# Optimization experiments

Hardware: AMD Instinct MI355X
Metric: run time of the kernel (lower is better)

The kernel has to match this reference:

```python
import jax, jax.numpy as jnp
import numpy as np


def setup_inputs() -> dict:
    key = jax.random.key(0)
    kh, ks, kwi, kwo, kcw = jax.random.split(key, 5)
    B = 2048        # decode batch (one token per request)
    H = 2048        # hidden_size
    K = 4           # conv kernel; L_cache = K - 1 = 3
    P = 8192        # req_to_token_pool size
    hidden_states = jax.random.normal(kh, (B, H), dtype=jnp.float32)
    conv_state = jax.random.normal(ks, (P, H, K - 1), dtype=jnp.float32)
    # unique, in-range pool slots (index_copy_ semantics need uniqueness)
    req_pool_indices = jnp.arange(B, dtype=jnp.int32)
    w_in = jax.random.normal(kwi, (3 * H, H), dtype=jnp.float32) * 0.02
    w_out = jax.random.normal(kwo, (H, H), dtype=jnp.float32) * 0.02
    conv_w = jax.random.normal(kcw, (H, K), dtype=jnp.float32) * 0.2
    return {
        "hidden_states": hidden_states,
        "conv_state": conv_state,
        "req_pool_indices": req_pool_indices,
        "w_in": w_in,
        "w_out": w_out,
        "conv_w": conv_w,
    }


def reference(hidden_states, conv_state, req_pool_indices, w_in, w_out, conv_w):
    """Lfm2ShortConv._forward_decode (conv_bias=False).

    Returns (y, new_conv_state) where new_conv_state is the scattered cache.
    """
    idx = req_pool_indices.astype(jnp.int32)
    # in_proj: [B, H] @ [H, 3H] -> [B, 3H]
    proj = hidden_states @ w_in.T
    B_gate, C_gate, x = jnp.split(proj, 3, axis=-1)
    Bx = B_gate * x                                  # [B, H]
    cur = conv_state[idx]                            # gather: [B, H, K-1]
    # sliding window: [old state (K-1 taps), newest token] -> [B, H, K]
    conv_in = jnp.concatenate([cur, Bx[:, :, None]], axis=-1)
    # depthwise causal conv as mul-sum over taps
    conv_out = jnp.einsum("bhk,hk->bh", conv_in, conv_w)
    y = (C_gate * conv_out) @ w_out.T                # [B, H]
    # scatter updated window (drop oldest tap)
    new_conv_state = conv_state.at[idx].set(conv_in[:, :, 1:])
    return y, new_conv_state
```

## Files before the change

### kernel.cpp

```cpp
#include <hip/hip_runtime.h>
#include <hip/hip_bf16.h>


typedef __bf16 bf16x8 __attribute__((ext_vector_type(8)));
typedef float f32x4 __attribute__((ext_vector_type(4)));

__device__ __forceinline__ unsigned short f2bf(float f) {
    union { float f; unsigned int u; } c; c.f = f;
    unsigned int u = c.u;
    u = u + 0x7FFFu + ((u >> 16) & 1u);
    return (unsigned short)(u >> 16);
}
__device__ __forceinline__ float bf2f(unsigned short u) {
    union { unsigned int i; float f; } c; c.i = ((unsigned int)u) << 16;
    return c.f;
}

__global__ void prep(const float4* __restrict__ hs, const float4* __restrict__ wi,
                     const float4* __restrict__ wo,
                     ushort4* __restrict__ hs_bf, ushort4* __restrict__ wi_bf,
                     ushort4* __restrict__ wo_bf,
                     int* __restrict__ inv, int P,
                     int n1, int n2, int n3) {
    int i = blockIdx.x * blockDim.x + threadIdx.x;
    if (i < P) inv[i] = -1;
    const float4* s; ushort4* d; int j = i;
    if (j < n1)            { s = hs; d = hs_bf; }
    else if ((j -= n1) < n2) { s = wi; d = wi_bf; }
    else if ((j -= n2) < n3) { s = wo; d = wo_bf; }
    else return;
    float4 v = s[j];
    ushort4 o; o.x = f2bf(v.x); o.y = f2bf(v.y); o.z = f2bf(v.z); o.w = f2bf(v.w);
    d[j] = o;
}

__global__ void scatter_inv(const int* __restrict__ idx, int* __restrict__ inv, int B) {
    int b = blockIdx.x * blockDim.x + threadIdx.x;
    if (b < B) inv[idx[b]] = b;
}


#define GTILE 128
#define GBK 64

__device__ __forceinline__ void gl_lds16(const unsigned short* g, unsigned short* l) {
    __builtin_amdgcn_global_load_lds(
        (const __attribute__((address_space(1))) unsigned int*)g,
        (__attribute__((address_space(3))) unsigned int*)l,
        16, 0, 0);
}

template<int OUTBF16>
__global__ __launch_bounds__(256) void gemm_bt(
    const unsigned short* __restrict__ A,
    const unsigned short* __restrict__ B,
    void* __restrict__ Cv,
    int M, int N, int K, int ksplit)
{
    __shared__ __align__(16) unsigned short Asm[GTILE * GBK];
    __shared__ __align__(16) unsigned short Bsm[GTILE * GBK];

    const int tid  = threadIdx.x;
    const int lane = tid & 63;
    const int wave = tid >> 6;
    const int quad = lane >> 4;
    const int l16  = lane & 15;

    const int bm = blockIdx.y * GTILE;
    const int bn = blockIdx.x * GTILE;
    const int kb = blockIdx.z * ksplit;

    const int wm = (wave >> 1) * 64;
    const int wn = (wave & 1) * 64;

    f32x4 acc[4][4] = {};

    const int sr = tid >> 3;
    const int scsw = (((tid & 7) ^ (sr & 7)) * 8);
    const unsigned short* Ag[4];
    const unsigned short* Bg[4];
#pragma unroll
    for (int k4 = 0; k4 < 4; k4++) {
        Ag[k4] = A + (size_t)(bm + k4 * 32 + sr) * K + scsw;
        Bg[k4] = B + (size_t)(bn + k4 * 32 + sr) * K + scsw;
    }

    for (int kt = kb; kt < kb + ksplit; kt += GBK) {
        __syncthreads();
#pragma unroll
        for (int k4 = 0; k4 < 4; k4++) {
            gl_lds16(Ag[k4] + kt, Asm + k4 * 2048 + wave * 512);
            gl_lds16(Bg[k4] + kt, Bsm + k4 * 2048 + wave * 512);
        }
        __syncthreads();

#pragma unroll
        for (int kk = 0; kk < 2; kk++) {
            bf16x8 a[4], b[4];
            const int csw = (kk * 32 + quad * 8) ^ ((l16 & 7) * 8);
#pragma unroll
            for (int i = 0; i < 4; i++)
                a[i] = *(const bf16x8*)&Asm[(wm + i * 16 + l16) * GBK + csw];
#pragma unroll
            for (int j = 0; j < 4; j++)
                b[j] = *(const bf16x8*)&Bsm[(wn + j * 16 + l16) * GBK + csw];
#pragma unroll
            for (int i = 0; i < 4; i++)
#pragma unroll
                for (int j = 0; j < 4; j++)
                    acc[i][j] = __builtin_amdgcn_mfma_f32_16x16x32_bf16(
                        a[i], b[j], acc[i][j], 0, 0, 0);
        }
    }

#pragma unroll
    for (int i = 0; i < 4; i++) {
#pragma unroll
        for (int j = 0; j < 4; j++) {
#pragma unroll
            for (int r = 0; r < 4; r++) {
                int row = bm + wm + i * 16 + quad * 4 + r;
                int col = bn + wn + j * 16 + l16;
                if (OUTBF16) {
                    ((unsigned short*)Cv)[(size_t)row * N + col] = f2bf(acc[i][j][r]);
                } else {
                    float* Cp = (float*)Cv + (size_t)blockIdx.z * M * N;
                    Cp[(size_t)row * N + col] = acc[i][j][r];
                }
            }
        }
    }
}

__global__ void elemwise(const unsigned short* __restrict__ proj,
                         const float* __restrict__ cs_in,
                         const int* __restrict__ idx,
                         const float* __restrict__ conv_w,
                         float* __restrict__ state_out,
                         unsigned short* __restrict__ g_bf,
                         int B, int H, int hshift, int hmask)
{
    int t = blockIdx.x * blockDim.x + threadIdx.x;
    if (t >= B * H) return;
    int b = t >> hshift;
    int h = t & hmask;
    int slot = idx[b];
    size_t prow = (size_t)b * 3 * H;
    float Bg = bf2f(proj[prow + h]);
    float Cg = bf2f(proj[prow + H + h]);
    float xv = bf2f(proj[prow + 2 * H + h]);
    float bx = Bg * xv;
    const float* cs = cs_in + ((size_t)slot * H + h) * 3;
    float c0 = cs[0], c1 = cs[1], c2 = cs[2];
    float4 cw = *(const float4*)(conv_w + 4 * h);
    float co = c0 * cw.x + c1 * cw.y + c2 * cw.z + bx * cw.w;
    float* so = state_out + ((size_t)slot * H + h) * 3;
    so[0] = c1; so[1] = c2; so[2] = bx;
    g_bf[t] = f2bf(Cg * co);
}

__global__ __launch_bounds__(256) void writeback(
    const float* __restrict__ cs_in,
    const int* __restrict__ inv,
    float* __restrict__ cs_out,
    int HL)
{
    int p = blockIdx.x;
    if (inv[p] >= 0) return;
    const float4* s4 = (const float4*)(cs_in + (size_t)p * HL);
    float4* d4 = (float4*)(cs_out + (size_t)p * HL);
    int n4 = HL / 4;
    for (int f = threadIdx.x; f < n4; f += blockDim.x) d4[f] = s4[f];
}

__global__ void reduce2(const float4* __restrict__ p0, const float4* __restrict__ p1,
                        float4* __restrict__ y, int n4) {
    int i = blockIdx.x * blockDim.x + threadIdx.x;
    if (i >= n4) return;
    float4 a = p0[i], b = p1[i];
    float4 o; o.x = a.x + b.x; o.y = a.y + b.y; o.z = a.z + b.z; o.w = a.w + b.w;
    y[i] = o;
}

extern "C" void kernel_launch(void* const* d_in, const int* in_sizes, int n_in,
                              void* d_out, int out_size, void* d_ws, size_t ws_size,
                              hipStream_t stream) {
    const float* hs         = (const float*)d_in[0];
    const float* conv_state = (const float*)d_in[1];
    const int*   idx        = (const int*)d_in[2];
    const float* w_in       = (const float*)d_in[3];
    const float* w_out      = (const float*)d_in[4];
    const float* conv_w     = (const float*)d_in[5];

    const int B  = in_sizes[2];
    const int H  = in_sizes[0] / B;
    const int Kc = in_sizes[5] / H;
    const int Lc = Kc - 1;
    const int P  = (int)((long long)in_sizes[1] / ((long long)H * Lc));

    float* y_out     = (float*)d_out;
    float* state_out = y_out + (size_t)B * H;

    unsigned short* hs_bf    = (unsigned short*)d_ws;
    unsigned short* w_in_bf  = hs_bf + (size_t)B * H;
    unsigned short* w_out_bf = w_in_bf + (size_t)3 * H * H;
    unsigned short* proj_bf  = w_out_bf + (size_t)H * H;
    unsigned short* g_bf     = proj_bf + (size_t)B * 3 * H;
    float*          part     = (float*)(g_bf + (size_t)B * H);
    int*            inv      = (int*)(part + (size_t)2 * B * H);

    const int thr = 256;

    {
        int n1 = B * H / 4, n2 = 3 * H * H / 4, n3 = H * H / 4;
        int tot = n1 + n2 + n3;
        prep<<<(tot + thr - 1) / thr, thr, 0, stream>>>(
            (const float4*)hs, (const float4*)w_in, (const float4*)w_out,
            (ushort4*)hs_bf, (ushort4*)w_in_bf, (ushort4*)w_out_bf,
            inv, P, n1, n2, n3);
    }
    scatter_inv<<<(B + thr - 1) / thr, thr, 0, stream>>>(idx, inv, B);

    {
        dim3 grid(3 * H / GTILE, B / GTILE, 1);
        gemm_bt<1><<<grid, 256, 0, stream>>>(hs_bf, w_in_bf, proj_bf, B, 3 * H, H, H);
    }

    {
        int hshift = 0; while ((1 << hshift) < H) hshift++;
        int n = B * H;
        elemwise<<<(n + thr - 1) / thr, thr, 0, stream>>>(
            proj_bf, conv_state, idx, conv_w, state_out, g_bf, B, H, hshift, H - 1);
    }

    writeback<<<P, 256, 0, stream>>>(conv_state, inv, state_out, 3 * H);

    {
        dim3 grid(H / GTILE, B / GTILE, 2);
        gemm_bt<0><<<grid, 256, 0, stream>>>(g_bf, w_out_bf, part, B, H, H, H / 2);
        int n4 = B * H / 4;
        reduce2<<<(n4 + thr - 1) / thr, thr, 0, stream>>>(
            (const float4*)part, (const float4*)(part + (size_t)B * H),
            (float4*)y_out, n4);
    }
}
```

Measured before the change: 502.8 us.

## Fuse state writeback into in-proj GEMM and use atomic split-K for out-proj

The separate writeback kernel is removed. Every fifth block of the in_proj GEMM grid now copies the untouched conv_state slots, so that memory traffic overlaps with MFMA work. The out_proj GEMM switches to 4-way split-K with relaxed float atomics into y, which prep now zero-fills, and the partial buffer and reduce kernel are dropped. This cuts launches and partial-buffer traffic, at the cost of atomic contention, nondeterministic summation order, and copy blocks that may load-imbalance the GEMM.

```diff
diff --git a/kernel.cpp b/kernel.cpp
--- a/kernel.cpp
+++ b/kernel.cpp
@@ -20,14 +20,16 @@
                      const float4* __restrict__ wo,
                      ushort4* __restrict__ hs_bf, ushort4* __restrict__ wi_bf,
                      ushort4* __restrict__ wo_bf,
+                     float4* __restrict__ y,
                      int* __restrict__ inv, int P,
-                     int n1, int n2, int n3) {
+                     int n1, int n2, int n3, int n4) {
     int i = blockIdx.x * blockDim.x + threadIdx.x;
     if (i < P) inv[i] = -1;
     const float4* s; ushort4* d; int j = i;
     if (j < n1)            { s = hs; d = hs_bf; }
     else if ((j -= n1) < n2) { s = wi; d = wi_bf; }
     else if ((j -= n2) < n3) { s = wo; d = wo_bf; }
+    else if ((j -= n3) < n4) { float4 z = {0.f, 0.f, 0.f, 0.f}; y[j] = z; return; }
     else return;
     float4 v = s[j];
     ushort4 o; o.x = f2bf(v.x); o.y = f2bf(v.y); o.z = f2bf(v.z); o.w = f2bf(v.w);
@@ -50,15 +52,43 @@
         16, 0, 0);
 }
 
-template<int OUTBF16>
+template<int MODE>
 __global__ __launch_bounds__(256) void gemm_bt(
     const unsigned short* __restrict__ A,
     const unsigned short* __restrict__ B,
     void* __restrict__ Cv,
-    int M, int N, int K, int ksplit)
+    int M, int N, int K, int ksplit, int nbx,
+    const float* __restrict__ cs_in,
+    const int* __restrict__ inv,
+    float* __restrict__ cs_out,
+    int HL, int P, int NC)
 {
     __shared__ __align__(16) unsigned short Asm[GTILE * GBK];
     __shared__ __align__(16) unsigned short Bsm[GTILE * GBK];
+
+    int bm, bn, kb;
+    if (MODE == 1) {
+        int id = blockIdx.x;
+        int q = id / 5, r = id % 5;
+        if (r == 4) {
+            for (int p = q; p < P; p += NC) {
+                if (inv[p] >= 0) continue;
+                const float4* s4 = (const float4*)(cs_in + (size_t)p * HL);
+                float4* d4 = (float4*)(cs_out + (size_t)p * HL);
+#pragma unroll
+                for (int f = threadIdx.x; f < GTILE * 12; f += 256) d4[f] = s4[f];
+            }
+            return;
+        }
+        int gid = q * 4 + r;
+        bn = (gid % nbx) * GTILE;
+        bm = (gid / nbx) * GTILE;
+        kb = 0;
+    } else {
+        bn = blockIdx.x * GTILE;
+        bm = blockIdx.y * GTILE;
+        kb = blockIdx.z * ksplit;
+    }
 
     const int tid  = threadIdx.x;
     const int lane = tid & 63;
@@ -66,10 +96,6 @@
     const int quad = lane >> 4;
     const int l16  = lane & 15;
 
-    const int bm = blockIdx.y * GTILE;
-    const int bn = blockIdx.x * GTILE;
-    const int kb = blockIdx.z * ksplit;
-
     const int wm = (wave >> 1) * 64;
     const int wn = (wave & 1) * 64;
 
@@ -121,11 +147,13 @@
             for (int r = 0; r < 4; r++) {
                 int row = bm + wm + i * 16 + quad * 4 + r;
                 int col = bn + wn + j * 16 + l16;
-                if (OUTBF16) {
+                if (MODE == 1) {
                     ((unsigned short*)Cv)[(size_t)row * N + col] = f2bf(acc[i][j][r]);
                 } else {
-                    float* Cp = (float*)Cv + (size_t)blockIdx.z * M * N;
-                    Cp[(size_t)row * N + col] = acc[i][j][r];
+                    __hip_atomic_fetch_add((float*)Cv + (size_t)row * N + col,
+                                           acc[i][j][r],
+                                           __ATOMIC_RELAXED,
+                                           __HIP_MEMORY_SCOPE_AGENT);
                 }
             }
         }
@@ -159,29 +187,6 @@
     g_bf[t] = f2bf(Cg * co);
 }
 
-__global__ __launch_bounds__(256) void writeback(
-    const float* __restrict__ cs_in,
-    const int* __restrict__ inv,
-    float* __restrict__ cs_out,
-    int HL)
-{
-    int p = blockIdx.x;
-    if (inv[p] >= 0) return;
-    const float4* s4 = (const float4*)(cs_in + (size_t)p * HL);
-    float4* d4 = (float4*)(cs_out + (size_t)p * HL);
-    int n4 = HL / 4;
-    for (int f = threadIdx.x; f < n4; f += blockDim.x) d4[f] = s4[f];
-}
-
-__global__ void reduce2(const float4* __restrict__ p0, const float4* __restrict__ p1,
-                        float4* __restrict__ y, int n4) {
-    int i = blockIdx.x * blockDim.x + threadIdx.x;
-    if (i >= n4) return;
-    float4 a = p0[i], b = p1[i];
-    float4 o; o.x = a.x + b.x; o.y = a.y + b.y; o.z = a.z + b.z; o.w = a.w + b.w;
-    y[i] = o;
-}
-
 extern "C" void kernel_launch(void* const* d_in, const int* in_sizes, int n_in,
                               void* d_out, int out_size, void* d_ws, size_t ws_size,
                               hipStream_t stream) {
@@ -206,24 +211,27 @@
     unsigned short* w_out_bf = w_in_bf + (size_t)3 * H * H;
     unsigned short* proj_bf  = w_out_bf + (size_t)H * H;
     unsigned short* g_bf     = proj_bf + (size_t)B * 3 * H;
-    float*          part     = (float*)(g_bf + (size_t)B * H);
-    int*            inv      = (int*)(part + (size_t)2 * B * H);
+    int*            inv      = (int*)(g_bf + (size_t)B * H);
 
     const int thr = 256;
 
     {
-        int n1 = B * H / 4, n2 = 3 * H * H / 4, n3 = H * H / 4;
-        int tot = n1 + n2 + n3;
+        int n1 = B * H / 4, n2 = 3 * H * H / 4, n3 = H * H / 4, n4 = B * H / 4;
+        int tot = n1 + n2 + n3 + n4;
         prep<<<(tot + thr - 1) / thr, thr, 0, stream>>>(
             (const float4*)hs, (const float4*)w_in, (const float4*)w_out,
             (ushort4*)hs_bf, (ushort4*)w_in_bf, (ushort4*)w_out_bf,
-            inv, P, n1, n2, n3);
+            (float4*)y_out, inv, P, n1, n2, n3, n4);
     }
     scatter_inv<<<(B + thr - 1) / thr, thr, 0, stream>>>(idx, inv, B);
 
     {
-        dim3 grid(3 * H / GTILE, B / GTILE, 1);
-        gemm_bt<1><<<grid, 256, 0, stream>>>(hs_bf, w_in_bf, proj_bf, B, 3 * H, H, H);
+        int nbx = 3 * H / GTILE;
+        int NG  = nbx * (B / GTILE);
+        int NC  = NG / 4;
+        gemm_bt<1><<<NG + NC, 256, 0, stream>>>(
+            hs_bf, w_in_bf, proj_bf, B, 3 * H, H, H, nbx,
+            conv_state, inv, state_out, 3 * H, P, NC);
     }
 
     {
@@ -233,14 +241,10 @@
             proj_bf, conv_state, idx, conv_w, state_out, g_bf, B, H, hshift, H - 1);
     }
 
-    writeback<<<P, 256, 0, stream>>>(conv_state, inv, state_out, 3 * H);
-
-    {
-        dim3 grid(H / GTILE, B / GTILE, 2);
-        gemm_bt<0><<<grid, 256, 0, stream>>>(g_bf, w_out_bf, part, B, H, H, H / 2);
-        int n4 = B * H / 4;
-        reduce2<<<(n4 + thr - 1) / thr, thr, 0, stream>>>(
-            (const float4*)part, (const float4*)(part + (size_t)B * H),
-            (float4*)y_out, n4);
-    }
-}
+    {
+        dim3 grid(H / GTILE, B / GTILE, 4);
+        gemm_bt<0><<<grid, 256, 0, stream>>>(
+            g_bf, w_out_bf, y_out, B, H, H, H / 4, H / GTILE,
+            nullptr, nullptr, nullptr, 0, 0, 0);
+    }
+}
```

New measurement: 579.5 us. 15.3% more time.

## Fuse conv-state writeback copy into first GEMM grid and use split-K of four

Applied to the files above, without the earlier changes.

The standalone writeback kernel for untouched conv-state slots now runs inside the first GEMM launch: every fifth block copies pool rows while the other blocks compute tiles, so the memory-bound copy overlaps the matmul. The second GEMM moves from split-K 2 to split-K 4 with a four-way reduce, giving more blocks for occupancy. This costs double the partial-sum workspace traffic and makes the copy blocks compete with GEMM tiles for CUs.

```diff
diff --git a/kernel.cpp b/kernel.cpp
--- a/kernel.cpp
+++ b/kernel.cpp
@@ -50,30 +50,19 @@
         16, 0, 0);
 }
 
-template<int OUTBF16>
-__global__ __launch_bounds__(256) void gemm_bt(
-    const unsigned short* __restrict__ A,
-    const unsigned short* __restrict__ B,
-    void* __restrict__ Cv,
-    int M, int N, int K, int ksplit)
-{
-    __shared__ __align__(16) unsigned short Asm[GTILE * GBK];
-    __shared__ __align__(16) unsigned short Bsm[GTILE * GBK];
-
+__device__ __forceinline__ void gemm_core(
+    const unsigned short* __restrict__ A, const unsigned short* __restrict__ B,
+    int K, int bm, int bn, int kb, int ksplit,
+    unsigned short* Asm, unsigned short* Bsm, f32x4 (&acc)[4][4])
+{
     const int tid  = threadIdx.x;
     const int lane = tid & 63;
     const int wave = tid >> 6;
     const int quad = lane >> 4;
     const int l16  = lane & 15;
 
-    const int bm = blockIdx.y * GTILE;
-    const int bn = blockIdx.x * GTILE;
-    const int kb = blockIdx.z * ksplit;
-
     const int wm = (wave >> 1) * 64;
     const int wn = (wave & 1) * 64;
-
-    f32x4 acc[4][4] = {};
 
     const int sr = tid >> 3;
     const int scsw = (((tid & 7) ^ (sr & 7)) * 8);
@@ -112,24 +101,92 @@
                         a[i], b[j], acc[i][j], 0, 0, 0);
         }
     }
-
-#pragma unroll
-    for (int i = 0; i < 4; i++) {
-#pragma unroll
-        for (int j = 0; j < 4; j++) {
-#pragma unroll
-            for (int r = 0; r < 4; r++) {
-                int row = bm + wm + i * 16 + quad * 4 + r;
+}
+
+__global__ __launch_bounds__(256) void gemm1_fused(
+    const unsigned short* __restrict__ A,
+    const unsigned short* __restrict__ B,
+    unsigned short* __restrict__ C,
+    int M, int N, int K, int nbx,
+    const float* __restrict__ cs_in,
+    const int* __restrict__ inv,
+    float* __restrict__ cs_out,
+    int HL, int P, int NC)
+{
+    __shared__ __align__(16) unsigned short Asm[GTILE * GBK];
+    __shared__ __align__(16) unsigned short Bsm[GTILE * GBK];
+
+    int id = blockIdx.x;
+    int q = id / 5, r = id % 5;
+    if (r == 4) {
+        int n4 = HL / 4;
+        for (int p = q; p < P; p += NC) {
+            if (inv[p] >= 0) continue;
+            const float4* s4 = (const float4*)(cs_in + (size_t)p * HL);
+            float4* d4 = (float4*)(cs_out + (size_t)p * HL);
+#pragma unroll 6
+            for (int f = threadIdx.x; f < n4; f += 256) d4[f] = s4[f];
+        }
+        return;
+    }
+    int gid = q * 4 + r;
+    int bn = (gid % nbx) * GTILE;
+    int bm = (gid / nbx) * GTILE;
+
+    f32x4 acc[4][4] = {};
+    gemm_core(A, B, K, bm, bn, 0, K, Asm, Bsm, acc);
+
+    const int lane = threadIdx.x & 63;
+    const int wave = threadIdx.x >> 6;
+    const int quad = lane >> 4;
+    const int l16  = lane & 15;
+    const int wm = (wave >> 1) * 64;
+    const int wn = (wave & 1) * 64;
+#pragma unroll
+    for (int i = 0; i < 4; i++)
+#pragma unroll
+        for (int j = 0; j < 4; j++)
+#pragma unroll
+            for (int rr = 0; rr < 4; rr++) {
+                int row = bm + wm + i * 16 + quad * 4 + rr;
                 int col = bn + wn + j * 16 + l16;
-                if (OUTBF16) {
-                    ((unsigned short*)Cv)[(size_t)row * N + col] = f2bf(acc[i][j][r]);
-                } else {
-                    float* Cp = (float*)Cv + (size_t)blockIdx.z * M * N;
-                    Cp[(size_t)row * N + col] = acc[i][j][r];
-                }
+                C[(size_t)row * N + col] = f2bf(acc[i][j][rr]);
             }
-        }
-    }
+}
+
+__global__ __launch_bounds__(256) void gemm2_split(
+    const unsigned short* __restrict__ A,
+    const unsigned short* __restrict__ B,
+    float* __restrict__ part,
+    int M, int N, int K, int ksplit)
+{
+    __shared__ __align__(16) unsigned short Asm[GTILE * GBK];
+    __shared__ __align__(16) unsigned short Bsm[GTILE * GBK];
+
+    int bn = blockIdx.x * GTILE;
+    int bm = blockIdx.y * GTILE;
+    int kb = blockIdx.z * ksplit;
+
+    f32x4 acc[4][4] = {};
+    gemm_core(A, B, K, bm, bn, kb, ksplit, Asm, Bsm, acc);
+
+    float* Cp = part + (size_t)blockIdx.z * M * N;
+    const int lane = threadIdx.x & 63;
+    const int wave = threadIdx.x >> 6;
+    const int quad = lane >> 4;
+    const int l16  = lane & 15;
+    const int wm = (wave >> 1) * 64;
+    const int wn = (wave & 1) * 64;
+#pragma unroll
+    for (int i = 0; i < 4; i++)
+#pragma unroll
+        for (int j = 0; j < 4; j++)
+#pragma unroll
+            for (int rr = 0; rr < 4; rr++) {
+                int row = bm + wm + i * 16 + quad * 4 + rr;
+                int col = bn + wn + j * 16 + l16;
+                Cp[(size_t)row * N + col] = acc[i][j][rr];
+            }
 }
 
 __global__ void elemwise(const unsigned short* __restrict__ proj,
@@ -159,26 +216,16 @@
     g_bf[t] = f2bf(Cg * co);
 }
 
-__global__ __launch_bounds__(256) void writeback(
-    const float* __restrict__ cs_in,
-    const int* __restrict__ inv,
-    float* __restrict__ cs_out,
-    int HL)
-{
-    int p = blockIdx.x;
-    if (inv[p] >= 0) return;
-    const float4* s4 = (const float4*)(cs_in + (size_t)p * HL);
-    float4* d4 = (float4*)(cs_out + (size_t)p * HL);
-    int n4 = HL / 4;
-    for (int f = threadIdx.x; f < n4; f += blockDim.x) d4[f] = s4[f];
-}
-
-__global__ void reduce2(const float4* __restrict__ p0, const float4* __restrict__ p1,
-                        float4* __restrict__ y, int n4) {
+__global__ void reduce4(const float4* __restrict__ p, float4* __restrict__ y,
+                        int n4) {
     int i = blockIdx.x * blockDim.x + threadIdx.x;
     if (i >= n4) return;
-    float4 a = p0[i], b = p1[i];
-    float4 o; o.x = a.x + b.x; o.y = a.y + b.y; o.z = a.z + b.z; o.w = a.w + b.w;
+    float4 a = p[i], b = p[i + n4], c = p[i + 2 * n4], d = p[i + 3 * n4];
+    float4 o;
+    o.x = (a.x + b.x) + (c.x + d.x);
+    o.y = (a.y + b.y) + (c.y + d.y);
+    o.z = (a.z + b.z) + (c.z + d.z);
+    o.w = (a.w + b.w) + (c.w + d.w);
     y[i] = o;
 }
 
@@ -207,7 +254,7 @@
     unsigned short* proj_bf  = w_out_bf + (size_t)H * H;
     unsigned short* g_bf     = proj_bf + (size_t)B * 3 * H;
     float*          part     = (float*)(g_bf + (size_t)B * H);
-    int*            inv      = (int*)(part + (size_t)2 * B * H);
+    int*            inv      = (int*)(part + (size_t)4 * B * H);
 
     const int thr = 256;
 
@@ -222,8 +269,12 @@
     scatter_inv<<<(B + thr - 1) / thr, thr, 0, stream>>>(idx, inv, B);
 
     {
-        dim3 grid(3 * H / GTILE, B / GTILE, 1);
-        gemm_bt<1><<<grid, 256, 0, stream>>>(hs_bf, w_in_bf, proj_bf, B, 3 * H, H, H);
+        int nbx = 3 * H / GTILE;
+        int NG  = nbx * (B / GTILE);
+        int NC  = NG / 4;
+        gemm1_fused<<<NG + NC, 256, 0, stream>>>(
+            hs_bf, w_in_bf, proj_bf, B, 3 * H, H, nbx,
+            conv_state, inv, state_out, 3 * H, P, NC);
     }
 
     {
@@ -233,14 +284,11 @@
             proj_bf, conv_state, idx, conv_w, state_out, g_bf, B, H, hshift, H - 1);
     }
 
-    writeback<<<P, 256, 0, stream>>>(conv_state, inv, state_out, 3 * H);
-
-    {
-        dim3 grid(H / GTILE, B / GTILE, 2);
-        gemm_bt<0><<<grid, 256, 0, stream>>>(g_bf, w_out_bf, part, B, H, H, H / 2);
+    {
+        dim3 grid(H / GTILE, B / GTILE, 4);
+        gemm2_split<<<grid, 256, 0, stream>>>(g_bf, w_out_bf, part, B, H, H, H / 4);
         int n4 = B * H / 4;
-        reduce2<<<(n4 + thr - 1) / thr, thr, 0, stream>>>(
-            (const float4*)part, (const float4*)(part + (size_t)B * H),
-            (float4*)y_out, n4);
-    }
-}
+        reduce4<<<(n4 + thr - 1) / thr, thr, 0, stream>>>(
+            (const float4*)part, (float4*)y_out, n4);
+    }
+}
```

New measurement: 528.0 us. 5.0% more time.

## Fuse in_proj GEMM with conv epilogue and writeback; split-K within gemm2 blocks

Applied to the files above, without the earlier changes.

The first GEMM now computes the B, C and x tiles for the same output columns in one block and applies the gating, depthwise conv and state scatter in registers. This removes the bf16 proj round trip through memory and the separate elementwise kernel. Every third block does the unused-slot state copy instead, so that copy overlaps with the GEMM. The second GEMM uses 512-thread blocks with two K-quarter groups reduced through LDS, which raises parallelism per block. The cost is that each GEMM1 block runs three full GEMMs serially and keeps 96 packed registers live, which may hurt occupancy.

```diff
diff --git a/kernel.cpp b/kernel.cpp
--- a/kernel.cpp
+++ b/kernel.cpp
@@ -50,127 +50,213 @@
         16, 0, 0);
 }
 
-template<int OUTBF16>
-__global__ __launch_bounds__(256) void gemm_bt(
+__device__ __forceinline__ void gemm_core(
+    const unsigned short* __restrict__ A, const unsigned short* __restrict__ B,
+    int K, int bm, int bn, int kb, int ksplit,
+    unsigned short* Asm, unsigned short* Bsm, f32x4 (&acc)[4][4], int tl)
+{
+    const int lane = tl & 63;
+    const int wave = tl >> 6;
+    const int quad = lane >> 4;
+    const int l16  = lane & 15;
+
+    const int wm = (wave >> 1) * 64;
+    const int wn = (wave & 1) * 64;
+
+    const int sr = tl >> 3;
+    const int scsw = (((tl & 7) ^ (sr & 7)) * 8);
+    const unsigned short* Ag[4];
+    const unsigned short* Bg[4];
+#pragma unroll
+    for (int k4 = 0; k4 < 4; k4++) {
+        Ag[k4] = A + (size_t)(bm + k4 * 32 + sr) * K + scsw;
+        Bg[k4] = B + (size_t)(bn + k4 * 32 + sr) * K + scsw;
+    }
+
+    for (int kt = kb; kt < kb + ksplit; kt += GBK) {
+        __syncthreads();
+#pragma unroll
+        for (int k4 = 0; k4 < 4; k4++) {
+            gl_lds16(Ag[k4] + kt, Asm + k4 * 2048 + wave * 512);
+            gl_lds16(Bg[k4] + kt, Bsm + k4 * 2048 + wave * 512);
+        }
+        __syncthreads();
+
+#pragma unroll
+        for (int kk = 0; kk < 2; kk++) {
+            bf16x8 a[4], b[4];
+            const int csw = (kk * 32 + quad * 8) ^ ((l16 & 7) * 8);
+#pragma unroll
+            for (int i = 0; i < 4; i++)
+                a[i] = *(const bf16x8*)&Asm[(wm + i * 16 + l16) * GBK + csw];
+#pragma unroll
+            for (int j = 0; j < 4; j++)
+                b[j] = *(const bf16x8*)&Bsm[(wn + j * 16 + l16) * GBK + csw];
+#pragma unroll
+            for (int i = 0; i < 4; i++)
+#pragma unroll
+                for (int j = 0; j < 4; j++)
+                    acc[i][j] = __builtin_amdgcn_mfma_f32_16x16x32_bf16(
+                        a[i], b[j], acc[i][j], 0, 0, 0);
+        }
+    }
+}
+
+__device__ __forceinline__ void pack_acc(const f32x4 (&acc)[4][4], unsigned int (&dst)[32]) {
+#pragma unroll
+    for (int i = 0; i < 4; i++)
+#pragma unroll
+        for (int j = 0; j < 4; j++) {
+            dst[(i * 4 + j) * 2 + 0] =
+                (unsigned int)f2bf(acc[i][j][0]) | ((unsigned int)f2bf(acc[i][j][1]) << 16);
+            dst[(i * 4 + j) * 2 + 1] =
+                (unsigned int)f2bf(acc[i][j][2]) | ((unsigned int)f2bf(acc[i][j][3]) << 16);
+        }
+}
+
+__global__ __launch_bounds__(256) void gemm1_fused3(
     const unsigned short* __restrict__ A,
-    const unsigned short* __restrict__ B,
-    void* __restrict__ Cv,
-    int M, int N, int K, int ksplit)
+    const unsigned short* __restrict__ Wb,
+    int H, int K,
+    const int* __restrict__ idx,
+    const float* __restrict__ conv_w,
+    const float* __restrict__ cs_in,
+    const int* __restrict__ inv,
+    float* __restrict__ state_out,
+    unsigned short* __restrict__ g_out,
+    int P, int NC)
 {
     __shared__ __align__(16) unsigned short Asm[GTILE * GBK];
     __shared__ __align__(16) unsigned short Bsm[GTILE * GBK];
 
-    const int tid  = threadIdx.x;
+    const int id = blockIdx.x;
+    const int q = id / 3, r = id % 3;
+    const int HL = 3 * H;
+    if (r == 2) {
+        int n4 = HL / 4;
+        for (int p = q; p < P; p += NC) {
+            if (inv[p] >= 0) continue;
+            const float4* s4 = (const float4*)(cs_in + (size_t)p * HL);
+            float4* d4 = (float4*)(state_out + (size_t)p * HL);
+#pragma unroll 6
+            for (int f = threadIdx.x; f < n4; f += 256) d4[f] = s4[f];
+        }
+        return;
+    }
+    const int gid = q * 2 + r;
+    const int bm = (gid >> 4) * GTILE;
+    const int bh = (gid & 15) * GTILE;
+
+    const int tid = threadIdx.x;
+
+    unsigned int pb[32], pc[32], px[32];
+    {
+        f32x4 acc[4][4] = {};
+        gemm_core(A, Wb, K, bm, bh, 0, K, Asm, Bsm, acc, tid);
+        pack_acc(acc, pb);
+    }
+    {
+        f32x4 acc[4][4] = {};
+        gemm_core(A, Wb + (size_t)H * K, K, bm, bh, 0, K, Asm, Bsm, acc, tid);
+        pack_acc(acc, pc);
+    }
+    {
+        f32x4 acc[4][4] = {};
+        gemm_core(A, Wb + (size_t)2 * H * K, K, bm, bh, 0, K, Asm, Bsm, acc, tid);
+        pack_acc(acc, px);
+    }
+
     const int lane = tid & 63;
     const int wave = tid >> 6;
     const int quad = lane >> 4;
     const int l16  = lane & 15;
-
-    const int bm = blockIdx.y * GTILE;
-    const int bn = blockIdx.x * GTILE;
-    const int kb = blockIdx.z * ksplit;
-
     const int wm = (wave >> 1) * 64;
     const int wn = (wave & 1) * 64;
+#pragma unroll
+    for (int i = 0; i < 4; i++) {
+#pragma unroll
+        for (int j = 0; j < 4; j++) {
+            const int hcol = bh + wn + j * 16 + l16;
+            const float4 cw = *(const float4*)(conv_w + 4 * hcol);
+            const int k2 = (i * 4 + j) * 2;
+#pragma unroll
+            for (int rr = 0; rr < 4; rr++) {
+                const int brow = bm + wm + i * 16 + quad * 4 + rr;
+                const unsigned int ub = pb[k2 + (rr >> 1)];
+                const unsigned int uc = pc[k2 + (rr >> 1)];
+                const unsigned int ux = px[k2 + (rr >> 1)];
+                const int sh = (rr & 1) * 16;
+                const float Bg = bf2f((unsigned short)(ub >> sh));
+                const float Cg = bf2f((unsigned short)(uc >> sh));
+                const float xv = bf2f((unsigned short)(ux >> sh));
+                const float bx = Bg * xv;
+                const int slot = idx[brow];
+                const float* cs = cs_in + ((size_t)slot * H + hcol) * 3;
+                const float c0 = cs[0], c1 = cs[1], c2 = cs[2];
+                const float co = c0 * cw.x + c1 * cw.y + c2 * cw.z + bx * cw.w;
+                float* so = state_out + ((size_t)slot * H + hcol) * 3;
+                so[0] = c1; so[1] = c2; so[2] = bx;
+                g_out[(size_t)brow * H + hcol] = f2bf(Cg * co);
+            }
+        }
+    }
+}
+
+__global__ __launch_bounds__(512) void gemm2_ws(
+    const unsigned short* __restrict__ A,
+    const unsigned short* __restrict__ B,
+    float* __restrict__ part,
+    int M, int N, int K)
+{
+    __shared__ __align__(16) unsigned short smem[4 * GTILE * GBK];
+
+    const int tid = threadIdx.x;
+    const int grp = tid >> 8;
+    const int tl  = tid & 255;
+
+    const int bn = blockIdx.x * GTILE;
+    const int bm = blockIdx.y * GTILE;
+    const int kq = K >> 2;
+    const int kb = blockIdx.z * (K >> 1) + grp * kq;
+
+    unsigned short* As = smem + grp * 2 * GTILE * GBK;
+    unsigned short* Bs = As + GTILE * GBK;
 
     f32x4 acc[4][4] = {};
-
-    const int sr = tid >> 3;
-    const int scsw = (((tid & 7) ^ (sr & 7)) * 8);
-    const unsigned short* Ag[4];
-    const unsigned short* Bg[4];
-#pragma unroll
-    for (int k4 = 0; k4 < 4; k4++) {
-        Ag[k4] = A + (size_t)(bm + k4 * 32 + sr) * K + scsw;
-        Bg[k4] = B + (size_t)(bn + k4 * 32 + sr) * K + scsw;
-    }
-
-    for (int kt = kb; kt < kb + ksplit; kt += GBK) {
-        __syncthreads();
-#pragma unroll
-        for (int k4 = 0; k4 < 4; k4++) {
-            gl_lds16(Ag[k4] + kt, Asm + k4 * 2048 + wave * 512);
-            gl_lds16(Bg[k4] + kt, Bsm + k4 * 2048 + wave * 512);
-        }
-        __syncthreads();
-
-#pragma unroll
-        for (int kk = 0; kk < 2; kk++) {
-            bf16x8 a[4], b[4];
-            const int csw = (kk * 32 + quad * 8) ^ ((l16 & 7) * 8);
-#pragma unroll
-            for (int i = 0; i < 4; i++)
-                a[i] = *(const bf16x8*)&Asm[(wm + i * 16 + l16) * GBK + csw];
+    gemm_core(A, B, K, bm, bn, kb, kq, As, Bs, acc, tl);
+
+    __syncthreads();
+    float* stash = (float*)smem;
+    if (grp == 1) {
+#pragma unroll
+        for (int i = 0; i < 4; i++)
 #pragma unroll
             for (int j = 0; j < 4; j++)
-                b[j] = *(const bf16x8*)&Bsm[(wn + j * 16 + l16) * GBK + csw];
-#pragma unroll
-            for (int i = 0; i < 4; i++)
-#pragma unroll
-                for (int j = 0; j < 4; j++)
-                    acc[i][j] = __builtin_amdgcn_mfma_f32_16x16x32_bf16(
-                        a[i], b[j], acc[i][j], 0, 0, 0);
-        }
-    }
-
-#pragma unroll
-    for (int i = 0; i < 4; i++) {
-#pragma unroll
-        for (int j = 0; j < 4; j++) {
-#pragma unroll
-            for (int r = 0; r < 4; r++) {
-                int row = bm + wm + i * 16 + quad * 4 + r;
-                int col = bn + wn + j * 16 + l16;
-                if (OUTBF16) {
-                    ((unsigned short*)Cv)[(size_t)row * N + col] = f2bf(acc[i][j][r]);
-                } else {
-                    float* Cp = (float*)Cv + (size_t)blockIdx.z * M * N;
-                    Cp[(size_t)row * N + col] = acc[i][j][r];
+#pragma unroll
+                for (int rr = 0; rr < 4; rr++)
+                    stash[((i * 4 + j) * 4 + rr) * 256 + tl] = acc[i][j][rr];
+    }
+    __syncthreads();
+    if (grp == 0) {
+        float* Cp = part + (size_t)blockIdx.z * M * N;
+        const int lane = tl & 63;
+        const int wave = tl >> 6;
+        const int quad = lane >> 4;
+        const int l16  = lane & 15;
+        const int wm = (wave >> 1) * 64;
+        const int wn = (wave & 1) * 64;
+#pragma unroll
+        for (int i = 0; i < 4; i++)
+#pragma unroll
+            for (int j = 0; j < 4; j++)
+#pragma unroll
+                for (int rr = 0; rr < 4; rr++) {
+                    int row = bm + wm + i * 16 + quad * 4 + rr;
+                    int col = bn + wn + j * 16 + l16;
+                    Cp[(size_t)row * N + col] =
+                        acc[i][j][rr] + stash[((i * 4 + j) * 4 + rr) * 256 + tl];
                 }
-            }
-        }
-    }
-}
-
-__global__ void elemwise(const unsigned short* __restrict__ proj,
-                         const float* __restrict__ cs_in,
-                         const int* __restrict__ idx,
-                         const float* __restrict__ conv_w,
-                         float* __restrict__ state_out,
-                         unsigned short* __restrict__ g_bf,
-                         int B, int H, int hshift, int hmask)
-{
-    int t = blockIdx.x * blockDim.x + threadIdx.x;
-    if (t >= B * H) return;
-    int b = t >> hshift;
-    int h = t & hmask;
-    int slot = idx[b];
-    size_t prow = (size_t)b * 3 * H;
-    float Bg = bf2f(proj[prow + h]);
-    float Cg = bf2f(proj[prow + H + h]);
-    float xv = bf2f(proj[prow + 2 * H + h]);
-    float bx = Bg * xv;
-    const float* cs = cs_in + ((size_t)slot * H + h) * 3;
-    float c0 = cs[0], c1 = cs[1], c2 = cs[2];
-    float4 cw = *(const float4*)(conv_w + 4 * h);
-    float co = c0 * cw.x + c1 * cw.y + c2 * cw.z + bx * cw.w;
-    float* so = state_out + ((size_t)slot * H + h) * 3;
-    so[0] = c1; so[1] = c2; so[2] = bx;
-    g_bf[t] = f2bf(Cg * co);
-}
-
-__global__ __launch_bounds__(256) void writeback(
-    const float* __restrict__ cs_in,
-    const int* __restrict__ inv,
-    float* __restrict__ cs_out,
-    int HL)
-{
-    int p = blockIdx.x;
-    if (inv[p] >= 0) return;
-    const float4* s4 = (const float4*)(cs_in + (size_t)p * HL);
-    float4* d4 = (float4*)(cs_out + (size_t)p * HL);
-    int n4 = HL / 4;
-    for (int f = threadIdx.x; f < n4; f += blockDim.x) d4[f] = s4[f];
+    }
 }
 
 __global__ void reduce2(const float4* __restrict__ p0, const float4* __restrict__ p1,
@@ -204,8 +290,7 @@
     unsigned short* hs_bf    = (unsigned short*)d_ws;
     unsigned short* w_in_bf  = hs_bf + (size_t)B * H;
     unsigned short* w_out_bf = w_in_bf + (size_t)3 * H * H;
-    unsigned short* proj_bf  = w_out_bf + (size_t)H * H;
-    unsigned short* g_bf     = proj_bf + (size_t)B * 3 * H;
+    unsigned short* g_bf     = w_out_bf + (size_t)H * H;
     float*          part     = (float*)(g_bf + (size_t)B * H);
     int*            inv      = (int*)(part + (size_t)2 * B * H);
 
@@ -222,22 +307,16 @@
     scatter_inv<<<(B + thr - 1) / thr, thr, 0, stream>>>(idx, inv, B);
 
     {
-        dim3 grid(3 * H / GTILE, B / GTILE, 1);
-        gemm_bt<1><<<grid, 256, 0, stream>>>(hs_bf, w_in_bf, proj_bf, B, 3 * H, H, H);
-    }
-
-    {
-        int hshift = 0; while ((1 << hshift) < H) hshift++;
-        int n = B * H;
-        elemwise<<<(n + thr - 1) / thr, thr, 0, stream>>>(
-            proj_bf, conv_state, idx, conv_w, state_out, g_bf, B, H, hshift, H - 1);
-    }
-
-    writeback<<<P, 256, 0, stream>>>(conv_state, inv, state_out, 3 * H);
+        int ncomp = (B / GTILE) * (H / GTILE);
+        int NC    = ncomp / 2;
+        gemm1_fused3<<<ncomp + NC, 256, 0, stream>>>(
+            hs_bf, w_in_bf, H, H, idx, conv_w, conv_state, inv,
+            state_out, g_bf, P, NC);
+    }
 
     {
         dim3 grid(H / GTILE, B / GTILE, 2);
-        gemm_bt<0><<<grid, 256, 0, stream>>>(g_bf, w_out_bf, part, B, H, H, H / 2);
+        gemm2_ws<<<grid, 512, 0, stream>>>(g_bf, w_out_bf, part, B, H, H);
         int n4 = B * H / 4;
         reduce2<<<(n4 + thr - 1) / thr, thr, 0, stream>>>(
             (const float4*)part, (const float4*)(part + (size_t)B * H),
```

Measured after the change: 624.1 us. +24.1%, slower.
